# Kernel tuning notes

Measured on AMD Instinct MI355X. Metric: run time of the kernel, lower is better.

Reference implementation:

```python
import jax, jax.numpy as jnp
import numpy as np

LEARN_PERCENT = 0.5


def setup_inputs() -> dict:
    key = jax.random.key(0)
    k1, k2 = jax.random.split(key)
    out = jax.random.normal(k1, (8192, 8192), dtype=jnp.float32)
    y = jax.random.normal(k2, (8192, 8192), dtype=jnp.float32)
    return {"out": out, "y": y}


def reference(out, y):
    # per-sample MSE: mean over all non-batch dims (nn.MSELoss default 'mean')
    B = out.shape[0]
    diff = out - y
    per_sample = jnp.mean(diff.reshape(B, -1) ** 2, axis=1)  # [B]
    k = int(B * LEARN_PERCENT)
    top_vals, _ = jax.lax.top_k(per_sample, k)  # largest=True, as torch.topk
    return jnp.sum(top_vals)
```

## Files before the change

### kernel.cpp

```cpp
#include <hip/hip_runtime.h>
#include <hip/hip_bf16.h>

#define K_SEL 4096
#define BINS 4096

__global__ __launch_bounds__(256) void row_mse_kernel(const float4* __restrict__ o4,
                                                      const float4* __restrict__ y4,
                                                      float* __restrict__ per) {
    const int row = blockIdx.x;
    const int tid = threadIdx.x;
    const size_t base = (size_t)row * 2048;

    float4 a[8], b[8];
    #pragma unroll
    for (int p = 0; p < 8; ++p) {
        a[p] = o4[base + tid + p * 256];
        b[p] = y4[base + tid + p * 256];
    }
    __builtin_amdgcn_sched_barrier(0);

    float acc = 0.0f;
    #pragma unroll
    for (int p = 0; p < 8; ++p) {
        float d0 = a[p].x - b[p].x;
        float d1 = a[p].y - b[p].y;
        float d2 = a[p].z - b[p].z;
        float d3 = a[p].w - b[p].w;
        acc = fmaf(d0, d0, acc);
        acc = fmaf(d1, d1, acc);
        acc = fmaf(d2, d2, acc);
        acc = fmaf(d3, d3, acc);
    }

    for (int off = 32; off > 0; off >>= 1) acc += __shfl_down(acc, off, 64);

    __shared__ float wsum[4];
    const int lane = tid & 63;
    const int wid = tid >> 6;
    if (lane == 0) wsum[wid] = acc;
    __syncthreads();
    if (tid == 0) {
        per[row] = (wsum[0] + wsum[1] + wsum[2] + wsum[3]) * (1.0f / 8192.0f);
    }
}

__global__ __launch_bounds__(1024) void topk_sum_kernel(const float* __restrict__ per,
                                                        float* __restrict__ out) {
    const int tid = threadIdx.x;
    const int lane = tid & 63;
    const int wid = tid >> 6;

    float v[8];
    #pragma unroll
    for (int p = 0; p < 8; ++p) v[p] = per[tid + p * 1024];

    float mn = v[0], mx = v[0];
    #pragma unroll
    for (int p = 1; p < 8; ++p) { mn = fminf(mn, v[p]); mx = fmaxf(mx, v[p]); }
    for (int off = 32; off > 0; off >>= 1) {
        mn = fminf(mn, __shfl_down(mn, off, 64));
        mx = fmaxf(mx, __shfl_down(mx, off, 64));
    }
    __shared__ float wmn[16], wmx[16];
    __shared__ float s_lo, s_hi, s_T;
    __shared__ int s_bin, s_kkb;
    if (lane == 0) { wmn[wid] = mn; wmx[wid] = mx; }
    __syncthreads();
    if (tid == 0) {
        float a = wmn[0], b = wmx[0];
        for (int i = 1; i < 16; ++i) { a = fminf(a, wmn[i]); b = fmaxf(b, wmx[i]); }
        s_lo = a; s_hi = b;
    }
    __syncthreads();
    const float lo = s_lo, hi = s_hi;

    float T;
    __shared__ unsigned hist[BINS];
    __shared__ float cand[1024];
    __shared__ unsigned ccnt;

    if (hi <= lo) {
        T = lo;
    } else {
        const float scale = (float)BINS / (hi - lo);
        const float w = (hi - lo) * (1.0f / (float)BINS);

        #pragma unroll
        for (int i = 0; i < BINS / 1024; ++i) hist[tid + i * 1024] = 0;
        __syncthreads();
        #pragma unroll
        for (int p = 0; p < 8; ++p) {
            int idx = (int)((v[p] - lo) * scale);
            idx = idx < 0 ? 0 : (idx > BINS - 1 ? BINS - 1 : idx);
            atomicAdd(&hist[idx], 1u);
        }
        __syncthreads();

        const int g = 1023 - tid;
        unsigned c = hist[4 * g] + hist[4 * g + 1] + hist[4 * g + 2] + hist[4 * g + 3];
        unsigned x = c;
        for (int off = 1; off < 64; off <<= 1) {
            unsigned t2 = __shfl_up(x, off, 64);
            if (lane >= off) x += t2;
        }
        __shared__ unsigned wtot[16];
        if (lane == 63) wtot[wid] = x;
        __syncthreads();
        unsigned basec = 0;
        for (int i = 0; i < wid; ++i) basec += wtot[i];
        const unsigned incl = basec + x;

        if (incl >= K_SEL && (incl - c) < K_SEL) {
            unsigned cum = incl - c;
            for (int b = 4 * g + 3; b >= 4 * g; --b) {
                unsigned hb = hist[b];
                if (cum + hb >= K_SEL) {
                    s_bin = b;
                    s_kkb = (int)(K_SEL - cum);
                    break;
                }
                cum += hb;
            }
        }
        __syncthreads();
        const int bin = s_bin;
        const int kkb = s_kkb;

        if (tid == 0) ccnt = 0;
        __syncthreads();
        #pragma unroll
        for (int p = 0; p < 8; ++p) {
            int idx = (int)((v[p] - lo) * scale);
            idx = idx < 0 ? 0 : (idx > BINS - 1 ? BINS - 1 : idx);
            if (idx == bin) {
                unsigned a = atomicAdd(&ccnt, 1u);
                if (a < 1024) cand[a] = v[p];
            }
        }
        __syncthreads();

        if (tid == 0) {
            int n = (int)(ccnt < 1024u ? ccnt : 1024u);
            float thr;
            if (n > 0 && n <= 64 && kkb <= n) {
                thr = cand[0];
                for (int e = 0; e < kkb; ++e) {
                    float best = -1e30f; int bi = 0;
                    for (int i = 0; i < n; ++i) {
                        float cc = cand[i];
                        if (cc > best) { best = cc; bi = i; }
                    }
                    cand[bi] = -1e30f;
                    thr = best;
                }
            } else {
                thr = lo + (float)(bin + 1) * w;
            }
            s_T = thr;
        }
        __syncthreads();
        T = s_T;
    }

    float ssum = 0.0f, cgt = 0.0f;
    #pragma unroll
    for (int p = 0; p < 8; ++p) {
        if (v[p] > T) { ssum += v[p]; cgt += 1.0f; }
    }
    for (int off = 32; off > 0; off >>= 1) {
        ssum += __shfl_down(ssum, off, 64);
        cgt += __shfl_down(cgt, off, 64);
    }
    __shared__ float wss[16], wcg[16];
    if (lane == 0) { wss[wid] = ssum; wcg[wid] = cgt; }
    __syncthreads();
    if (tid == 0) {
        float ts = 0.0f, tc = 0.0f;
        for (int i = 0; i < 16; ++i) { ts += wss[i]; tc += wcg[i]; }
        out[0] = ts + ((float)K_SEL - tc) * T;
    }
}

extern "C" void kernel_launch(void* const* d_in, const int* in_sizes, int n_in,
                              void* d_out, int out_size, void* d_ws, size_t ws_size,
                              hipStream_t stream) {
    const float* o = (const float*)d_in[0];
    const float* y = (const float*)d_in[1];
    float* per = (float*)d_ws;
    float* out = (float*)d_out;

    row_mse_kernel<<<8192, 256, 0, stream>>>((const float4*)o, (const float4*)y, per);
    topk_sum_kernel<<<1, 1024, 0, stream>>>(per, out);
}
```

Before: 100.5 us.

## Process four rows per block with double-buffered register prefetch of half-rows

```diff
diff --git a/kernel.cpp b/kernel.cpp
--- a/kernel.cpp
+++ b/kernel.cpp
@@ -1,46 +1,90 @@
 #include <hip/hip_runtime.h>
 #include <hip/hip_bf16.h>
 
+#define NROWS 8192
+#define RPB 4
+#define NBLK (NROWS / RPB)
 #define K_SEL 4096
 #define BINS 4096
 
 __global__ __launch_bounds__(256) void row_mse_kernel(const float4* __restrict__ o4,
                                                       const float4* __restrict__ y4,
                                                       float* __restrict__ per) {
-    const int row = blockIdx.x;
     const int tid = threadIdx.x;
-    const size_t base = (size_t)row * 2048;
-
-    float4 a[8], b[8];
-    #pragma unroll
-    for (int p = 0; p < 8; ++p) {
-        a[p] = o4[base + tid + p * 256];
-        b[p] = y4[base + tid + p * 256];
-    }
-    __builtin_amdgcn_sched_barrier(0);
-
-    float acc = 0.0f;
-    #pragma unroll
-    for (int p = 0; p < 8; ++p) {
-        float d0 = a[p].x - b[p].x;
-        float d1 = a[p].y - b[p].y;
-        float d2 = a[p].z - b[p].z;
-        float d3 = a[p].w - b[p].w;
-        acc = fmaf(d0, d0, acc);
-        acc = fmaf(d1, d1, acc);
-        acc = fmaf(d2, d2, acc);
-        acc = fmaf(d3, d3, acc);
-    }
-
-    for (int off = 32; off > 0; off >>= 1) acc += __shfl_down(acc, off, 64);
-
-    __shared__ float wsum[4];
     const int lane = tid & 63;
     const int wid = tid >> 6;
-    if (lane == 0) wsum[wid] = acc;
-    __syncthreads();
-    if (tid == 0) {
-        per[row] = (wsum[0] + wsum[1] + wsum[2] + wsum[3]) * (1.0f / 8192.0f);
+    const int row0 = blockIdx.x * RPB;
+
+    __shared__ float wsum[2][4];
+
+    float4 Aa[4], Ab[4], Ba[4], Bb[4];
+
+    {
+        const size_t cb = (size_t)row0 * 2048 + tid;
+        #pragma unroll
+        for (int p = 0; p < 4; ++p) Aa[p] = o4[cb + p * 256];
+        #pragma unroll
+        for (int p = 0; p < 4; ++p) Ab[p] = y4[cb + p * 256];
+    }
+
+    float acc = 0.0f;
+    #pragma unroll
+    for (int c = 0; c < 2 * RPB; ++c) {
+        if (c + 1 < 2 * RPB) {
+            const int nr = row0 + ((c + 1) >> 1);
+            const size_t cb = (size_t)nr * 2048 + ((c + 1) & 1) * 1024 + tid;
+            if ((c & 1) == 0) {
+                #pragma unroll
+                for (int p = 0; p < 4; ++p) Ba[p] = o4[cb + p * 256];
+                #pragma unroll
+                for (int p = 0; p < 4; ++p) Bb[p] = y4[cb + p * 256];
+            } else {
+                #pragma unroll
+                for (int p = 0; p < 4; ++p) Aa[p] = o4[cb + p * 256];
+                #pragma unroll
+                for (int p = 0; p < 4; ++p) Ab[p] = y4[cb + p * 256];
+            }
+        }
+        __builtin_amdgcn_sched_barrier(0);
+
+        if ((c & 1) == 0) {
+            #pragma unroll
+            for (int p = 0; p < 4; ++p) {
+                float d0 = Aa[p].x - Ab[p].x;
+                float d1 = Aa[p].y - Ab[p].y;
+                float d2 = Aa[p].z - Ab[p].z;
+                float d3 = Aa[p].w - Ab[p].w;
+                acc = fmaf(d0, d0, acc);
+                acc = fmaf(d1, d1, acc);
+                acc = fmaf(d2, d2, acc);
+                acc = fmaf(d3, d3, acc);
+            }
+        } else {
+            #pragma unroll
+            for (int p = 0; p < 4; ++p) {
+                float d0 = Ba[p].x - Bb[p].x;
+                float d1 = Ba[p].y - Bb[p].y;
+                float d2 = Ba[p].z - Bb[p].z;
+                float d3 = Ba[p].w - Bb[p].w;
+                acc = fmaf(d0, d0, acc);
+                acc = fmaf(d1, d1, acc);
+                acc = fmaf(d2, d2, acc);
+                acc = fmaf(d3, d3, acc);
+            }
+        }
+
+        if (c & 1) {
+            const int r = c >> 1;
+            const int bank = r & 1;
+            for (int off = 32; off > 0; off >>= 1) acc += __shfl_down(acc, off, 64);
+            if (lane == 0) wsum[bank][wid] = acc;
+            __syncthreads();
+            if (tid == 0) {
+                per[row0 + r] = (wsum[bank][0] + wsum[bank][1] +
+                                 wsum[bank][2] + wsum[bank][3]) * (1.0f / 8192.0f);
+            }
+            acc = 0.0f;
+        }
     }
 }
 
@@ -189,6 +233,6 @@
     float* per = (float*)d_ws;
     float* out = (float*)d_out;
 
-    row_mse_kernel<<<8192, 256, 0, stream>>>((const float4*)o, (const float4*)y, per);
+    row_mse_kernel<<<NBLK, 256, 0, stream>>>((const float4*)o, (const float4*)y, per);
     topk_sum_kernel<<<1, 1024, 0, stream>>>(per, out);
 }
```

Result: slower. 106.1 us (+5.5%).
